# Optimization experiments

Hardware: AMD Instinct MI355X
Metric: run time of the kernel (lower is better)

## Reference

```python
import jax, jax.numpy as jnp
import numpy as np

B, N, D, H = 4, 1024, 1024, 16
DH = D // H
NEG_BIG = -2.0**32 + 1.0  # padding value from the torch code


def setup_inputs() -> dict:
    key = jax.random.key(0)
    ks = jax.random.split(key, 12)
    inp = {
        "x": jax.random.normal(ks[0], (B, N, D), dtype=jnp.float32),
        "key_padding_mask": jnp.zeros((B, N), dtype=bool),  # True = padded
        # attention projections (nn.Linear, bias=False): y = x @ W.T
        "Wq": jax.random.normal(ks[1], (D, D), dtype=jnp.float32) * (D ** -0.5),
        "Wk": jax.random.normal(ks[2], (D, D), dtype=jnp.float32) * (D ** -0.5),
        "Wv": jax.random.normal(ks[3], (D, D), dtype=jnp.float32) * (D ** -0.5),
        # FFN
        "W1": jax.random.normal(ks[4], (D, D), dtype=jnp.float32) * (D ** -0.5),
        "b1": jnp.zeros((D,), dtype=jnp.float32),
        "W2": jax.random.normal(ks[5], (D, D), dtype=jnp.float32) * (D ** -0.5),
        "b2": jnp.zeros((D,), dtype=jnp.float32),
        # MaskedLayerNorm params
        "g1": jnp.ones((D,), dtype=jnp.float32),
        "beta1": jnp.zeros((D,), dtype=jnp.float32),
        "g2": jnp.ones((D,), dtype=jnp.float32),
        "beta2": jnp.zeros((D,), dtype=jnp.float32),
    }
    return inp


def masked_layer_norm(x, scale, bias, eps=1e-5):
    mean = jnp.mean(x, axis=-1, keepdims=True)
    var = jnp.mean(jnp.square(x - mean), axis=-1, keepdims=True)
    return (x - mean) * jax.lax.rsqrt(var + eps) * scale + bias


def _to_heads(t):
    # torch: cat(split(t, DH, dim=2), dim=0) -> head-major [H*B, N, DH]
    b, n, d = t.shape
    return t.reshape(b, n, H, DH).transpose(2, 0, 1, 3).reshape(H * b, n, DH)


def _from_heads(t, b):
    # torch: cat(split(t, B, dim=0), dim=2) -> [B, N, D]
    hb, n, dh = t.shape
    return t.reshape(H, b, n, dh).transpose(1, 2, 0, 3).reshape(b, n, H * dh)


def attention(x, key_padding_mask, Wq, Wk, Wv):
    b, n, d = x.shape
    Q = _to_heads(x @ Wq.T)  # (H*B, N, DH)
    K = _to_heads(x @ Wk.T)
    V = _to_heads(x @ Wv.T)

    scores = jnp.einsum("znd,zmd->znm", Q, K) / (DH ** 0.5)  # (H*B, N, N)

    # key masks: sign of sum|K| over feature dim, broadcast over query axis
    key_masks = jnp.sign(jnp.sum(jnp.abs(K), axis=-1))  # (H*B, N)
    scores = jnp.where(key_masks[:, None, :] == 0, jnp.full_like(scores, NEG_BIG), scores)

    # temporal mask, direction == FORWARD: mask[i, j] = (j > i)
    idx = jnp.arange(n)
    attn_mask = idx[None, :] > idx[:, None]  # sw_row > sw_col with ij meshgrid
    scores = scores + (1.0 - attn_mask.astype(scores.dtype)) * -10000.0

    # NOTE: original code calls F.softmax(outputs) with no dim on a 3D tensor;
    # torch's implicit-dim rule selects dim=0 for ndim==3. Replicated faithfully.
    attn = jax.nn.softmax(scores, axis=0)

    query_masks = jnp.sign(jnp.sum(jnp.abs(Q), axis=-1))  # (H*B, N)
    attn = attn * query_masks[:, :, None]
    # dropout p=0.0 -> identity

    out = jnp.einsum("znm,zmd->znd", attn, V)  # (H*B, N, DH)
    out = _from_heads(out, b)  # (B, N, D)
    out = out * (~key_padding_mask)[:, :, None].astype(out.dtype)
    return out


def reference(x, key_padding_mask, Wq, Wk, Wv, W1, b1, W2, b2, g1, beta1, g2, beta2):
    attn_out = attention(x, key_padding_mask, Wq, Wk, Wv)
    h = masked_layer_norm(x + attn_out, g1, beta1)  # layer_norm1
    ff = jax.nn.relu(h @ W1.T + b1) @ W2.T + b2  # fc (dropout p=0)
    valid = (~key_padding_mask)[:, :, None].astype(ff.dtype)
    ff = ff * valid
    out = masked_layer_norm(ff + h, g2, beta2)  # layer_norm2
    out = out * valid
    return out
```

## Files before the change

### kernel.cpp

```cpp
#include <hip/hip_runtime.h>
#include <math.h>

typedef unsigned short u16;
typedef unsigned char  u8;
typedef unsigned int   u32;
typedef __attribute__((ext_vector_type(8))) short bf16x8;
typedef __attribute__((ext_vector_type(4))) float f32x4;

#define NSEQ   1024
#define DMODEL 1024
#define ZTOT   64
#define LOG2E  1.4426950408889634f

typedef const __attribute__((address_space(1))) void* gp1;
typedef __attribute__((address_space(3))) void* lp3;

__device__ __forceinline__ void gload16(const void* g, void* l) {
    __builtin_amdgcn_global_load_lds((gp1)g, (lp3)l, 16, 0, 0);
}

__device__ __forceinline__ u16 f2bf(float f) {
    u32 u = __builtin_bit_cast(u32, f);
    return (u16)((u + 0x7FFFu + ((u >> 16) & 1u)) >> 16);
}

__device__ __forceinline__ u32 cvt_pk_bf16(float a, float b) {
    u32 r;
    asm("v_cvt_pk_bf16_f32 %0, %1, %2" : "=v"(r) : "v"(a), "v"(b));
    return r;
}

__launch_bounds__(256)
__global__ void cvt_bf16(const float* __restrict__ in, u16* __restrict__ out) {
    int i = (blockIdx.x * 256 + threadIdx.x) * 4;
    float4 v = *(const float4*)(in + i);
    uint2 o;
    o.x = cvt_pk_bf16(v.x, v.y);
    o.y = cvt_pk_bf16(v.z, v.w);
    *(uint2*)(out + i) = o;
}

struct P5 { const float* in[5]; u16* out[5]; };
__launch_bounds__(256)
__global__ void cvt_bf16_5(P5 p) {
    int which = blockIdx.x >> 10;
    int blk   = blockIdx.x & 1023;
    int i = (blk * 256 + threadIdx.x) * 4;
    float4 v = *(const float4*)(p.in[which] + i);
    uint2 o;
    o.x = cvt_pk_bf16(v.x, v.y);
    o.y = cvt_pk_bf16(v.z, v.w);
    *(uint2*)(p.out[which] + i) = o;
}

__launch_bounds__(256)
__global__ void rowmask2_bf(const u16* __restrict__ Kh, const u16* __restrict__ Qh,
                            float* __restrict__ km, float* __restrict__ qm) {
    int b = blockIdx.x;
    const u16* T = (b < 256) ? Kh : Qh;
    float* o = (b < 256) ? km : qm;
    int r = (b & 255) * 256 + threadIdx.x;
    const uint4* p = (const uint4*)(T + (size_t)r * 64);
    u32 acc = 0;
    #pragma unroll
    for (int i = 0; i < 8; i++) {
        uint4 q = p[i];
        acc |= (q.x | q.y | q.z | q.w) & 0x7fff7fffu;
    }
    o[r] = acc ? 1.f : 0.f;
}

__launch_bounds__(256)
__global__ void vt_km(u16* __restrict__ Vt, const float* __restrict__ km) {
    int idx = blockIdx.x * 256 + threadIdx.x;
    int e0 = idx * 8;
    int z = e0 >> 16;
    int tok = e0 & 1023;
    float4 ka = *(const float4*)(km + z * 1024 + tok);
    float4 kb = *(const float4*)(km + z * 1024 + tok + 4);
    uint4 v = *(uint4*)(Vt + e0);
    u32 m;
    m = (ka.x != 0.f ? 0x0000FFFFu : 0u) | (ka.y != 0.f ? 0xFFFF0000u : 0u); v.x &= m;
    m = (ka.z != 0.f ? 0x0000FFFFu : 0u) | (ka.w != 0.f ? 0xFFFF0000u : 0u); v.y &= m;
    m = (kb.x != 0.f ? 0x0000FFFFu : 0u) | (kb.y != 0.f ? 0xFFFF0000u : 0u); v.z &= m;
    m = (kb.z != 0.f ? 0x0000FFFFu : 0u) | (kb.w != 0.f ? 0xFFFF0000u : 0u); v.w &= m;
    *(uint4*)(Vt + e0) = v;
}

__launch_bounds__(256)
__global__ void gemm_qkv(const u16* __restrict__ A,
                         const u16* __restrict__ Wq, const u16* __restrict__ Wk,
                         const u16* __restrict__ Wv,
                         u16* __restrict__ Qh, u16* __restrict__ Kh, u16* __restrict__ Vt)
{
    __shared__ __align__(16) u16 lA[2][128 * 32];
    __shared__ __align__(16) u16 lB[2][128 * 32];
    const int tid = threadIdx.x, lane = tid & 63, w = tid >> 6;
    const int frow = lane & 15, koct = lane >> 4;
    const int sel = blockIdx.x >> 3;
    const int col0 = (blockIdx.x & 7) * 128, row0 = blockIdx.y * 128;
    const u16* B = (sel == 0) ? Wq : (sel == 1) ? Wk : Wv;
    const int wrow = (w >> 1) * 64, wcol = (w & 1) * 64;
    f32x4 acc[4][4] = {};

    auto stage = [&](int buf, int k0) {
        #pragma unroll
        for (int i = 0; i < 2; i++) {
            int p = tid + i * 256;
            int row = p >> 2, sl = p & 3, ssl = sl ^ ((row >> 1) & 3);
            gload16(A + (size_t)(row0 + row) * 1024 + k0 + ssl * 8, (char*)lA[buf] + p * 16);
        }
        #pragma unroll
        for (int i = 0; i < 2; i++) {
            int p = tid + i * 256;
            int row = p >> 2, sl = p & 3, ssl = sl ^ ((row >> 1) & 3);
            gload16(B + (size_t)(col0 + row) * 1024 + k0 + ssl * 8, (char*)lB[buf] + p * 16);
        }
    };

    stage(0, 0);
    __syncthreads();
    int buf = 0;
    for (int k0 = 0; k0 < 1024; k0 += 32) {
        if (k0 + 32 < 1024) stage(buf ^ 1, k0 + 32);
        __builtin_amdgcn_s_setprio(1);
        bf16x8 af[4], bf[4];
        #pragma unroll
        for (int i = 0; i < 4; i++) {
            int r = wrow + i * 16 + frow;
            int sl = koct ^ ((r >> 1) & 3);
            af[i] = *(const bf16x8*)((const char*)lA[buf] + r * 64 + sl * 16);
        }
        #pragma unroll
        for (int j = 0; j < 4; j++) {
            int r = wcol + j * 16 + frow;
            int sl = koct ^ ((r >> 1) & 3);
            bf[j] = *(const bf16x8*)((const char*)lB[buf] + r * 64 + sl * 16);
        }
        #pragma unroll
        for (int i = 0; i < 4; i++)
            #pragma unroll
            for (int j = 0; j < 4; j++)
                acc[i][j] = __builtin_amdgcn_mfma_f32_16x16x32_bf16(af[i], bf[j], acc[i][j], 0, 0, 0);
        __builtin_amdgcn_s_setprio(0);
        __syncthreads();
        buf ^= 1;
    }

    if (sel < 2) {
        const float scale = (sel == 0) ? 0.125f * LOG2E : 1.0f;
        u16* outp = (sel == 0) ? Qh : Kh;
        #pragma unroll
        for (int i = 0; i < 4; i++)
            #pragma unroll
            for (int j = 0; j < 4; j++)
                #pragma unroll
                for (int q = 0; q < 4; q++) {
                    int r = row0 + wrow + i * 16 + koct * 4 + q;
                    int c = col0 + wcol + j * 16 + frow;
                    float v = acc[i][j][q] * scale;
                    outp[(size_t)((c >> 6) * 4 + (r >> 10)) * 65536 +
                         (size_t)(r & 1023) * 64 + (c & 63)] = f2bf(v);
                }
    } else {
        #pragma unroll
        for (int i = 0; i < 4; i++) {
            int r0 = row0 + wrow + i * 16 + koct * 4;
            #pragma unroll
            for (int j = 0; j < 4; j++) {
                int c = col0 + wcol + j * 16 + frow;
                int z = (c >> 6) * 4 + (r0 >> 10);
                uint2 pk;
                pk.x = cvt_pk_bf16(acc[i][j][0], acc[i][j][1]);
                pk.y = cvt_pk_bf16(acc[i][j][2], acc[i][j][3]);
                *(uint2*)(Vt + (size_t)z * 65536 + (size_t)(c & 63) * 1024 + (r0 & 1023)) = pk;
            }
        }
    }
}

template <int MODE>
__launch_bounds__(256)
__global__ void gemm_bt(const u16* __restrict__ A, const u16* __restrict__ B,
                        const float* __restrict__ bias, void* __restrict__ outp)
{
    __shared__ __align__(16) u16 lA[2][128 * 64];
    __shared__ __align__(16) u16 lB[2][64 * 64];
    const int tid = threadIdx.x, lane = tid & 63, w = tid >> 6;
    const int frow = lane & 15, koct = lane >> 4;
    const int col0 = blockIdx.x * 64, row0 = blockIdx.y * 128;
    const int wrow = (w >> 1) * 64, wcol = (w & 1) * 32;
    f32x4 acc[4][2] = {};

    auto stage = [&](int buf, int k0) {
        #pragma unroll
        for (int i = 0; i < 4; i++) {
            int p = tid + i * 256;
            int row = p >> 3, sl = p & 7, ssl = sl ^ (row & 7);
            gload16(A + (size_t)(row0 + row) * 1024 + k0 + ssl * 8, (char*)lA[buf] + p * 16);
        }
        #pragma unroll
        for (int i = 0; i < 2; i++) {
            int p = tid + i * 256;
            int row = p >> 3, sl = p & 7, ssl = sl ^ (row & 7);
            gload16(B + (size_t)(col0 + row) * 1024 + k0 + ssl * 8, (char*)lB[buf] + p * 16);
        }
    };

    stage(0, 0);
    __syncthreads();
    int buf = 0;
    for (int k0 = 0; k0 < 1024; k0 += 64) {
        if (k0 + 64 < 1024) stage(buf ^ 1, k0 + 64);
        __builtin_amdgcn_s_setprio(1);
        #pragma unroll
        for (int ks = 0; ks < 2; ks++) {
            bf16x8 af[4], bf2[2];
            #pragma unroll
            for (int i = 0; i < 4; i++) {
                int r = wrow + i * 16 + frow;
                int sl = (ks * 4 + koct) ^ (r & 7);
                af[i] = *(const bf16x8*)((const char*)lA[buf] + r * 128 + sl * 16);
            }
            #pragma unroll
            for (int j = 0; j < 2; j++) {
                int r = wcol + j * 16 + frow;
                int sl = (ks * 4 + koct) ^ (r & 7);
                bf2[j] = *(const bf16x8*)((const char*)lB[buf] + r * 128 + sl * 16);
            }
            #pragma unroll
            for (int i = 0; i < 4; i++)
                #pragma unroll
                for (int j = 0; j < 2; j++)
                    acc[i][j] = __builtin_amdgcn_mfma_f32_16x16x32_bf16(af[i], bf2[j], acc[i][j], 0, 0, 0);
        }
        __builtin_amdgcn_s_setprio(0);
        __syncthreads();
        buf ^= 1;
    }

    #pragma unroll
    for (int i = 0; i < 4; i++)
        #pragma unroll
        for (int j = 0; j < 2; j++)
            #pragma unroll
            for (int q = 0; q < 4; q++) {
                int r = row0 + wrow + i * 16 + koct * 4 + q;
                int c = col0 + wcol + j * 16 + frow;
                float v = acc[i][j][q] + bias[c];
                if constexpr (MODE == 2) {
                    v = fmaxf(v, 0.f);
                    ((u16*)outp)[(size_t)r * 1024 + c] = f2bf(v);
                } else {
                    ((float*)outp)[(size_t)r * 1024 + c] = v;
                }
            }
}

__launch_bounds__(256)
__global__ void attn_pass1(const u16* __restrict__ Qh, const u16* __restrict__ Kh,
                           const float* __restrict__ km, float* __restrict__ partial)
{
    const int bid = blockIdx.x;
    const int mtzg = (bid & 7) * 8 + ((bid >> 3) & 7);
    const int m0 = (mtzg & 15) * 64, zg = mtzg >> 4;
    const int n0 = (bid >> 6) * 64;

    __shared__ __align__(16) u16 lQ[2][64 * 64];
    __shared__ __align__(16) u16 lK[2][64 * 64];
    const int tid = threadIdx.x, lane = tid & 63, w = tid >> 6;
    const int frow = lane & 15, koct = lane >> 4;
    const int wn = (w >> 1) * 32, wm = (w & 1) * 32;
    f32x4 ssum[2][2] = {};

    auto stage = [&](int buf, int z) {
        #pragma unroll
        for (int i = 0; i < 2; i++) {
            int p = tid + i * 256;
            int row = p >> 3, sl = p & 7, ssl = sl ^ (row & 7);
            gload16(Qh + (size_t)(z * NSEQ + n0 + row) * 64 + ssl * 8, (char*)lQ[buf] + p * 16);
            gload16(Kh + (size_t)(z * NSEQ + m0 + row) * 64 + ssl * 8, (char*)lK[buf] + p * 16);
        }
    };

    const int z0 = zg * 16;
    stage(0, z0);
    __syncthreads();
    int buf = 0;
    for (int zi = 0; zi < 16; zi++) {
        const int z = z0 + zi;
        if (zi < 15) stage(buf ^ 1, z + 1);
        f32x4 km4[2];
        #pragma unroll
        for (int j = 0; j < 2; j++)
            km4[j] = *(const f32x4*)(km + z * NSEQ + m0 + wm + j * 16 + koct * 4);
        f32x4 s[2][2] = {};
        __builtin_amdgcn_s_setprio(1);
        #pragma unroll
        for (int ks = 0; ks < 2; ks++) {
            bf16x8 a[2], b2[2];
            #pragma unroll
            for (int i = 0; i < 2; i++) {
                int r = wn + i * 16 + frow;
                int sl = (ks * 4 + koct) ^ (r & 7);
                a[i] = *(const bf16x8*)((const char*)lQ[buf] + r * 128 + sl * 16);
            }
            #pragma unroll
            for (int j = 0; j < 2; j++) {
                int r = wm + j * 16 + frow;
                int sl = (ks * 4 + koct) ^ (r & 7);
                b2[j] = *(const bf16x8*)((const char*)lK[buf] + r * 128 + sl * 16);
            }
            #pragma unroll
            for (int i = 0; i < 2; i++)
                #pragma unroll
                for (int j = 0; j < 2; j++)
                    s[i][j] = __builtin_amdgcn_mfma_f32_16x16x32_bf16(b2[j], a[i], s[i][j], 0, 0, 0);
        }
        __builtin_amdgcn_s_setprio(0);
        #pragma unroll
        for (int j = 0; j < 2; j++)
            #pragma unroll
            for (int i = 0; i < 2; i++)
                #pragma unroll
                for (int q = 0; q < 4; q++)
                    ssum[i][j][q] += __builtin_amdgcn_exp2f(s[i][j][q]) * km4[j][q];
        __syncthreads();
        buf ^= 1;
    }
    #pragma unroll
    for (int i = 0; i < 2; i++)
        #pragma unroll
        for (int j = 0; j < 2; j++) {
            int ng = n0 + wn + i * 16 + frow;
            int mg = m0 + wm + j * 16 + koct * 4;
            *(f32x4*)(partial + (size_t)zg * 1048576 + (size_t)ng * NSEQ + mg) = ssum[i][j];
        }
}

__launch_bounds__(256)
__global__ void sum_inv(const float* __restrict__ p, float* __restrict__ invS) {
    int i = (blockIdx.x * 256 + threadIdx.x) * 4;
    float4 a = *(const float4*)(p + i);
    float4 b = *(const float4*)(p + 1048576 + i);
    float4 c = *(const float4*)(p + 2097152 + i);
    float4 d = *(const float4*)(p + 3145728 + i);
    float4 r;
    float s;
    s = a.x + b.x + c.x + d.x; r.x = s > 0.f ? 1.f / s : 0.f;
    s = a.y + b.y + c.y + d.y; r.y = s > 0.f ? 1.f / s : 0.f;
    s = a.z + b.z + c.z + d.z; r.z = s > 0.f ? 1.f / s : 0.f;
    s = a.w + b.w + c.w + d.w; r.w = s > 0.f ? 1.f / s : 0.f;
    *(float4*)(invS + i) = r;
}

__launch_bounds__(256)
__global__ void attn_pass2(const u16* __restrict__ Qh, const u16* __restrict__ Kh,
                           const u16* __restrict__ Vt,
                           const float* __restrict__ qm, const float* __restrict__ invS,
                           const u8* __restrict__ pad, float* __restrict__ attn)
{
    const int bid = blockIdx.x;
    const int z  = (bid & 7) * 8 + ((bid >> 3) & 7);
    const int n0 = (bid >> 6) * 64;

    __shared__ __align__(16) u16 lK[2][64 * 64];
    __shared__ __align__(16) u16 lV[2][64 * 64];
    __shared__ __align__(16) u16 lP[64 * 64];
    const int tid = threadIdx.x, lane = tid & 63, w = tid >> 6;
    const int frow = lane & 15, koct = lane >> 4;
    const int hh = z >> 2, bb = z & 3;
    const int wrow = w * 16;
    const int nl_row = wrow + frow;
    const size_t inv_base = (size_t)(n0 + nl_row) * NSEQ;

    bf16x8 aq[2];
    #pragma unroll
    for (int ks = 0; ks < 2; ks++)
        aq[ks] = *(const bf16x8*)(Qh + (size_t)(z * NSEQ + n0 + nl_row) * 64 + ks * 32 + koct * 8);

    auto stage = [&](int buf, int m0) {
        #pragma unroll
        for (int i = 0; i < 2; i++) {
            int p = tid + i * 256;
            int row = p >> 3, sl = p & 7, ssl = sl ^ (row & 7);
            gload16(Kh + (size_t)(z * NSEQ + m0 + row) * 64 + ssl * 8, (char*)lK[buf] + p * 16);
            gload16(Vt + (size_t)z * 65536 + (size_t)row * 1024 + m0 + ssl * 8, (char*)lV[buf] + p * 16);
        }
    };

    f32x4 oacc[4] = {};
    f32x4 iv[4];
    #pragma unroll
    for (int j = 0; j < 4; j++)
        iv[j] = *(const f32x4*)(invS + inv_base + j * 16 + koct * 4);
    stage(0, 0);
    __syncthreads();
    int buf = 0;

    for (int mt = 0; mt < 16; mt++) {
        const int m0 = mt * 64;
        if (mt < 15) stage(buf ^ 1, m0 + 64);
        f32x4 ivn[4];
        if (mt < 15) {
            #pragma unroll
            for (int j = 0; j < 4; j++)
                ivn[j] = *(const f32x4*)(invS + inv_base + m0 + 64 + j * 16 + koct * 4);
        }
        f32x4 s[4] = {};
        __builtin_amdgcn_s_setprio(1);
        #pragma unroll
        for (int ks = 0; ks < 2; ks++) {
            bf16x8 kb[4];
            #pragma unroll
            for (int j = 0; j < 4; j++) {
                int r = j * 16 + frow;
                int sl = (ks * 4 + koct) ^ (r & 7);
                kb[j] = *(const bf16x8*)((const char*)lK[buf] + r * 128 + sl * 16);
            }
            #pragma unroll
            for (int j = 0; j < 4; j++)
                s[j] = __builtin_amdgcn_mfma_f32_16x16x32_bf16(kb[j], aq[ks], s[j], 0, 0, 0);
        }
        __builtin_amdgcn_s_setprio(0);
        #pragma unroll
        for (int j = 0; j < 4; j++) {
            float p0 = __builtin_amdgcn_exp2f(s[j][0]) * iv[j][0];
            float p1 = __builtin_amdgcn_exp2f(s[j][1]) * iv[j][1];
            float p2 = __builtin_amdgcn_exp2f(s[j][2]) * iv[j][2];
            float p3 = __builtin_amdgcn_exp2f(s[j][3]) * iv[j][3];
            uint2 pk;
            pk.x = cvt_pk_bf16(p0, p1);
            pk.y = cvt_pk_bf16(p2, p3);
            int slot = (j * 2 + (koct >> 1)) ^ (nl_row & 7);
            *(uint2*)((char*)lP + nl_row * 128 + slot * 16 + (koct & 1) * 8) = pk;
        }
        __builtin_amdgcn_s_setprio(1);
        #pragma unroll
        for (int ks = 0; ks < 2; ks++) {
            int sl = (ks * 4 + koct) ^ (nl_row & 7);
            bf16x8 pa = *(const bf16x8*)((const char*)lP + nl_row * 128 + sl * 16);
            bf16x8 vb[4];
            #pragma unroll
            for (int dj = 0; dj < 4; dj++) {
                int rr = dj * 16 + frow;
                int sv = (ks * 4 + koct) ^ (rr & 7);
                vb[dj] = *(const bf16x8*)((const char*)lV[buf] + rr * 128 + sv * 16);
            }
            #pragma unroll
            for (int dj = 0; dj < 4; dj++)
                oacc[dj] = __builtin_amdgcn_mfma_f32_16x16x32_bf16(pa, vb[dj], oacc[dj], 0, 0, 0);
        }
        __builtin_amdgcn_s_setprio(0);
        __syncthreads();
        buf ^= 1;
        #pragma unroll
        for (int j = 0; j < 4; j++) iv[j] = ivn[j];
    }

    #pragma unroll
    for (int q = 0; q < 4; q++) {
        int ns = n0 + wrow + koct * 4 + q;
        float f = qm[z * NSEQ + ns] * (pad[bb * NSEQ + ns] ? 0.f : 1.f);
        #pragma unroll
        for (int dj = 0; dj < 4; dj++) {
            int d = dj * 16 + frow;
            attn[(size_t)(bb * NSEQ + ns) * DMODEL + hh * 64 + d] = oacc[dj][q] * f;
        }
    }
}

__launch_bounds__(256)
__global__ void ln_kernel(const float* __restrict__ A, const float* __restrict__ Bv,
                          const float* __restrict__ g, const float* __restrict__ beta,
                          const u8* __restrict__ pad, int mode,
                          float* __restrict__ out, u16* __restrict__ outb)
{
    const int row = blockIdx.x, tid = threadIdx.x;
    const int lane = tid & 63, wv = tid >> 6;
    const float valid = pad[row] ? 0.f : 1.f;
    __shared__ float red[4];

    float4 va = *(const float4*)(A + (size_t)row * 1024 + tid * 4);
    float4 vb = *(const float4*)(Bv + (size_t)row * 1024 + tid * 4);
    float v[4];
    if (mode == 0) {
        v[0] = va.x + vb.x; v[1] = va.y + vb.y; v[2] = va.z + vb.z; v[3] = va.w + vb.w;
    } else {
        v[0] = va.x * valid + vb.x; v[1] = va.y * valid + vb.y;
        v[2] = va.z * valid + vb.z; v[3] = va.w * valid + vb.w;
    }
    float s = v[0] + v[1] + v[2] + v[3];
    #pragma unroll
    for (int off = 32; off > 0; off >>= 1) s += __shfl_down(s, off, 64);
    if (lane == 0) red[wv] = s;
    __syncthreads();
    float mean = (red[0] + red[1] + red[2] + red[3]) * (1.f / 1024.f);
    float sq = 0.f;
    #pragma unroll
    for (int k = 0; k < 4; k++) { float d = v[k] - mean; sq += d * d; }
    __syncthreads();
    #pragma unroll
    for (int off = 32; off > 0; off >>= 1) sq += __shfl_down(sq, off, 64);
    if (lane == 0) red[wv] = sq;
    __syncthreads();
    float var = (red[0] + red[1] + red[2] + red[3]) * (1.f / 1024.f);
    float rstd = rsqrtf(var + 1e-5f);
    float osc = (mode == 0) ? 1.f : valid;
    #pragma unroll
    for (int k = 0; k < 4; k++) {
        int c = tid * 4 + k;
        float o = ((v[k] - mean) * rstd * g[c] + beta[c]) * osc;
        out[(size_t)row * 1024 + c] = o;
        if (outb) outb[(size_t)row * 1024 + c] = f2bf(o);
    }
}

extern "C" void kernel_launch(void* const* d_in, const int* in_sizes, int n_in,
                              void* d_out, int out_size, void* d_ws, size_t ws_size,
                              hipStream_t stream)
{
    const float* x   = (const float*)d_in[0];
    const u8*    pad = (const u8*)d_in[1];
    const float* Wq  = (const float*)d_in[2];
    const float* Wk  = (const float*)d_in[3];
    const float* Wv  = (const float*)d_in[4];
    const float* W1  = (const float*)d_in[5];
    const float* b1  = (const float*)d_in[6];
    const float* W2  = (const float*)d_in[7];
    const float* b2  = (const float*)d_in[8];
    const float* g1  = (const float*)d_in[9];
    const float* be1 = (const float*)d_in[10];
    const float* g2  = (const float*)d_in[11];
    const float* be2 = (const float*)d_in[12];
    float* out = (float*)d_out;

    u16* xb   = (u16*)d_ws;
    u16* Wqb  = xb   + 4194304;
    u16* Wkb  = Wqb  + 1048576;
    u16* Wvb  = Wkb  + 1048576;
    u16* W1b  = Wvb  + 1048576;
    u16* W2b  = W1b  + 1048576;
    u16* Qh   = W2b  + 1048576;
    u16* Kh   = Qh   + 4194304;
    u16* Vt   = Kh   + 4194304;
    u16* hb   = Vt   + 4194304;
    u16* ff1b = hb   + 4194304;
    float* km      = (float*)(ff1b + 4194304);
    float* qm      = km      + 65536;
    float* partial = qm      + 65536;
    float* invS    = partial + 4194304;
    float* h       = invS    + 1048576;

    cvt_bf16<<<4096, 256, 0, stream>>>(x, xb);
    P5 p5;
    p5.in[0] = Wq; p5.in[1] = Wk; p5.in[2] = Wv; p5.in[3] = W1; p5.in[4] = W2;
    p5.out[0] = Wqb; p5.out[1] = Wkb; p5.out[2] = Wvb; p5.out[3] = W1b; p5.out[4] = W2b;
    cvt_bf16_5<<<5120, 256, 0, stream>>>(p5);

    gemm_qkv<<<dim3(24, 32), 256, 0, stream>>>(xb, Wqb, Wkb, Wvb, Qh, Kh, Vt);

    rowmask2_bf<<<512, 256, 0, stream>>>(Kh, Qh, km, qm);
    vt_km<<<4096, 256, 0, stream>>>(Vt, km);

    attn_pass1<<<1024, 256, 0, stream>>>(Qh, Kh, km, partial);
    sum_inv<<<1024, 256, 0, stream>>>(partial, invS);
    attn_pass2<<<1024, 256, 0, stream>>>(Qh, Kh, Vt, qm, invS, pad, out);

    ln_kernel<<<4096, 256, 0, stream>>>(x, out, g1, be1, pad, 0, h, hb);

    gemm_bt<2><<<dim3(16, 32), 256, 0, stream>>>(hb,   W1b, b1, ff1b);
    gemm_bt<3><<<dim3(16, 32), 256, 0, stream>>>(ff1b, W2b, b2, out);

    ln_kernel<<<4096, 256, 0, stream>>>(out, h, g2, be2, pad, 1, out, nullptr);
}
```

Baseline: 200.2 us.

## Drop LDS staging in attention passes; give each wave independent tiles

Both attention passes stop staging Q/K/V tiles through shared memory with double buffering and block barriers. Instead, each wave reads its MFMA operands straight from global memory (relying on L1/L2) and owns its own 32x32 score tile (pass1) or 32-query tile (pass2, which now uses 512 blocks and a per-wave P buffer). The goal is to remove barrier stalls and LDS traffic and to let waves run independently. The cost is more global/L2 load traffic, since operands are no longer shared between the waves of a block, and unswizzled direct loads that may be less coalesced.

```diff
diff --git a/kernel.cpp b/kernel.cpp
--- a/kernel.cpp
+++ b/kernel.cpp
@@ -261,63 +261,42 @@
 __global__ void attn_pass1(const u16* __restrict__ Qh, const u16* __restrict__ Kh,
                            const float* __restrict__ km, float* __restrict__ partial)
 {
-    const int bid = blockIdx.x;
-    const int mtzg = (bid & 7) * 8 + ((bid >> 3) & 7);
-    const int m0 = (mtzg & 15) * 64, zg = mtzg >> 4;
-    const int n0 = (bid >> 6) * 64;
-
-    __shared__ __align__(16) u16 lQ[2][64 * 64];
-    __shared__ __align__(16) u16 lK[2][64 * 64];
     const int tid = threadIdx.x, lane = tid & 63, w = tid >> 6;
     const int frow = lane & 15, koct = lane >> 4;
-    const int wn = (w >> 1) * 32, wm = (w & 1) * 32;
+    const int bid = blockIdx.x;
+    const int c = bid & 7;
+    const int local = (bid >> 3) * 4 + w;
+    const int zg = c >> 1;
+    const int m0 = ((c & 1) * 16 + (local & 15)) * 32;
+    const int n0 = (local >> 4) * 32;
+
     f32x4 ssum[2][2] = {};
-
-    auto stage = [&](int buf, int z) {
-        #pragma unroll
-        for (int i = 0; i < 2; i++) {
-            int p = tid + i * 256;
-            int row = p >> 3, sl = p & 7, ssl = sl ^ (row & 7);
-            gload16(Qh + (size_t)(z * NSEQ + n0 + row) * 64 + ssl * 8, (char*)lQ[buf] + p * 16);
-            gload16(Kh + (size_t)(z * NSEQ + m0 + row) * 64 + ssl * 8, (char*)lK[buf] + p * 16);
-        }
-    };
-
     const int z0 = zg * 16;
-    stage(0, z0);
-    __syncthreads();
-    int buf = 0;
-    for (int zi = 0; zi < 16; zi++) {
-        const int z = z0 + zi;
-        if (zi < 15) stage(buf ^ 1, z + 1);
-        f32x4 km4[2];
-        #pragma unroll
-        for (int j = 0; j < 2; j++)
-            km4[j] = *(const f32x4*)(km + z * NSEQ + m0 + wm + j * 16 + koct * 4);
+    for (int z = z0; z < z0 + 16; z++) {
+        const u16* Qz = Qh + (size_t)z * 65536;
+        const u16* Kz = Kh + (size_t)z * 65536;
         f32x4 s[2][2] = {};
         __builtin_amdgcn_s_setprio(1);
         #pragma unroll
         for (int ks = 0; ks < 2; ks++) {
-            bf16x8 a[2], b2[2];
-            #pragma unroll
-            for (int i = 0; i < 2; i++) {
-                int r = wn + i * 16 + frow;
-                int sl = (ks * 4 + koct) ^ (r & 7);
-                a[i] = *(const bf16x8*)((const char*)lQ[buf] + r * 128 + sl * 16);
-            }
-            #pragma unroll
-            for (int j = 0; j < 2; j++) {
-                int r = wm + j * 16 + frow;
-                int sl = (ks * 4 + koct) ^ (r & 7);
-                b2[j] = *(const bf16x8*)((const char*)lK[buf] + r * 128 + sl * 16);
-            }
+            bf16x8 a[2], kb[2];
+            #pragma unroll
+            for (int i = 0; i < 2; i++)
+                a[i] = *(const bf16x8*)(Qz + (size_t)(n0 + i * 16 + frow) * 64 + ks * 32 + koct * 8);
+            #pragma unroll
+            for (int j = 0; j < 2; j++)
+                kb[j] = *(const bf16x8*)(Kz + (size_t)(m0 + j * 16 + frow) * 64 + ks * 32 + koct * 8);
             #pragma unroll
             for (int i = 0; i < 2; i++)
                 #pragma unroll
                 for (int j = 0; j < 2; j++)
-                    s[i][j] = __builtin_amdgcn_mfma_f32_16x16x32_bf16(b2[j], a[i], s[i][j], 0, 0, 0);
+                    s[i][j] = __builtin_amdgcn_mfma_f32_16x16x32_bf16(kb[j], a[i], s[i][j], 0, 0, 0);
         }
         __builtin_amdgcn_s_setprio(0);
+        f32x4 km4[2];
+        #pragma unroll
+        for (int j = 0; j < 2; j++)
+            km4[j] = *(const f32x4*)(km + z * NSEQ + m0 + j * 16 + koct * 4);
         #pragma unroll
         for (int j = 0; j < 2; j++)
             #pragma unroll
@@ -325,15 +304,13 @@
                 #pragma unroll
                 for (int q = 0; q < 4; q++)
                     ssum[i][j][q] += __builtin_amdgcn_exp2f(s[i][j][q]) * km4[j][q];
-        __syncthreads();
-        buf ^= 1;
     }
     #pragma unroll
     for (int i = 0; i < 2; i++)
         #pragma unroll
         for (int j = 0; j < 2; j++) {
-            int ng = n0 + wn + i * 16 + frow;
-            int mg = m0 + wm + j * 16 + koct * 4;
+            int ng = n0 + i * 16 + frow;
+            int mg = m0 + j * 16 + koct * 4;
             *(f32x4*)(partial + (size_t)zg * 1048576 + (size_t)ng * NSEQ + mg) = ssum[i][j];
         }
 }
@@ -360,114 +337,97 @@
                            const float* __restrict__ qm, const float* __restrict__ invS,
                            const u8* __restrict__ pad, float* __restrict__ attn)
 {
-    const int bid = blockIdx.x;
-    const int z  = (bid & 7) * 8 + ((bid >> 3) & 7);
-    const int n0 = (bid >> 6) * 64;
-
-    __shared__ __align__(16) u16 lK[2][64 * 64];
-    __shared__ __align__(16) u16 lV[2][64 * 64];
-    __shared__ __align__(16) u16 lP[64 * 64];
+    __shared__ __align__(16) u16 lP[4][32 * 64];
     const int tid = threadIdx.x, lane = tid & 63, w = tid >> 6;
     const int frow = lane & 15, koct = lane >> 4;
+    const int bid = blockIdx.x;
+    const int local = (bid >> 3) * 4 + w;
+    const int z  = (bid & 7) * 8 + (local >> 5);
+    const int n0 = (local & 31) * 32;
     const int hh = z >> 2, bb = z & 3;
-    const int wrow = w * 16;
-    const int nl_row = wrow + frow;
-    const size_t inv_base = (size_t)(n0 + nl_row) * NSEQ;
-
-    bf16x8 aq[2];
-    #pragma unroll
-    for (int ks = 0; ks < 2; ks++)
-        aq[ks] = *(const bf16x8*)(Qh + (size_t)(z * NSEQ + n0 + nl_row) * 64 + ks * 32 + koct * 8);
-
-    auto stage = [&](int buf, int m0) {
-        #pragma unroll
-        for (int i = 0; i < 2; i++) {
-            int p = tid + i * 256;
-            int row = p >> 3, sl = p & 7, ssl = sl ^ (row & 7);
-            gload16(Kh + (size_t)(z * NSEQ + m0 + row) * 64 + ssl * 8, (char*)lK[buf] + p * 16);
-            gload16(Vt + (size_t)z * 65536 + (size_t)row * 1024 + m0 + ssl * 8, (char*)lV[buf] + p * 16);
-        }
-    };
-
-    f32x4 oacc[4] = {};
-    f32x4 iv[4];
-    #pragma unroll
-    for (int j = 0; j < 4; j++)
-        iv[j] = *(const f32x4*)(invS + inv_base + j * 16 + koct * 4);
-    stage(0, 0);
-    __syncthreads();
-    int buf = 0;
+    char* lPw = (char*)&lP[w][0];
+
+    const u16* Kz = Kh + (size_t)z * 65536;
+    const u16* Vz = Vt + (size_t)z * 65536;
+
+    bf16x8 aq[2][2];
+    #pragma unroll
+    for (int i = 0; i < 2; i++)
+        #pragma unroll
+        for (int ks = 0; ks < 2; ks++)
+            aq[i][ks] = *(const bf16x8*)(Qh + (size_t)z * 65536 +
+                                         (size_t)(n0 + i * 16 + frow) * 64 + ks * 32 + koct * 8);
+
+    f32x4 oacc[2][4] = {};
 
     for (int mt = 0; mt < 16; mt++) {
         const int m0 = mt * 64;
-        if (mt < 15) stage(buf ^ 1, m0 + 64);
-        f32x4 ivn[4];
-        if (mt < 15) {
-            #pragma unroll
-            for (int j = 0; j < 4; j++)
-                ivn[j] = *(const f32x4*)(invS + inv_base + m0 + 64 + j * 16 + koct * 4);
-        }
-        f32x4 s[4] = {};
+        f32x4 s[2][4] = {};
         __builtin_amdgcn_s_setprio(1);
         #pragma unroll
         for (int ks = 0; ks < 2; ks++) {
             bf16x8 kb[4];
             #pragma unroll
+            for (int j = 0; j < 4; j++)
+                kb[j] = *(const bf16x8*)(Kz + (size_t)(m0 + j * 16 + frow) * 64 + ks * 32 + koct * 8);
+            #pragma unroll
+            for (int i = 0; i < 2; i++)
+                #pragma unroll
+                for (int j = 0; j < 4; j++)
+                    s[i][j] = __builtin_amdgcn_mfma_f32_16x16x32_bf16(kb[j], aq[i][ks], s[i][j], 0, 0, 0);
+        }
+        __builtin_amdgcn_s_setprio(0);
+        #pragma unroll
+        for (int i = 0; i < 2; i++) {
+            const size_t inv_base = (size_t)(n0 + i * 16 + frow) * NSEQ;
+            const int r = i * 16 + frow;
+            #pragma unroll
             for (int j = 0; j < 4; j++) {
-                int r = j * 16 + frow;
+                int mg = m0 + j * 16 + koct * 4;
+                f32x4 iv = *(const f32x4*)(invS + inv_base + mg);
+                float p0 = __builtin_amdgcn_exp2f(s[i][j][0]) * iv[0];
+                float p1 = __builtin_amdgcn_exp2f(s[i][j][1]) * iv[1];
+                float p2 = __builtin_amdgcn_exp2f(s[i][j][2]) * iv[2];
+                float p3 = __builtin_amdgcn_exp2f(s[i][j][3]) * iv[3];
+                uint2 pk;
+                pk.x = cvt_pk_bf16(p0, p1);
+                pk.y = cvt_pk_bf16(p2, p3);
+                int slot = (j * 2 + (koct >> 1)) ^ (r & 7);
+                *(uint2*)(lPw + r * 128 + slot * 16 + (koct & 1) * 8) = pk;
+            }
+        }
+        __builtin_amdgcn_s_setprio(1);
+        #pragma unroll
+        for (int ks = 0; ks < 2; ks++) {
+            bf16x8 vb[4];
+            #pragma unroll
+            for (int dj = 0; dj < 4; dj++)
+                vb[dj] = *(const bf16x8*)(Vz + (size_t)(dj * 16 + frow) * 1024 + m0 + ks * 32 + koct * 8);
+            #pragma unroll
+            for (int i = 0; i < 2; i++) {
+                const int r = i * 16 + frow;
                 int sl = (ks * 4 + koct) ^ (r & 7);
-                kb[j] = *(const bf16x8*)((const char*)lK[buf] + r * 128 + sl * 16);
-            }
-            #pragma unroll
-            for (int j = 0; j < 4; j++)
-                s[j] = __builtin_amdgcn_mfma_f32_16x16x32_bf16(kb[j], aq[ks], s[j], 0, 0, 0);
+                bf16x8 pa = *(const bf16x8*)(lPw + r * 128 + sl * 16);
+                #pragma unroll
+                for (int dj = 0; dj < 4; dj++)
+                    oacc[i][dj] = __builtin_amdgcn_mfma_f32_16x16x32_bf16(pa, vb[dj], oacc[i][dj], 0, 0, 0);
+            }
         }
         __builtin_amdgcn_s_setprio(0);
-        #pragma unroll
-        for (int j = 0; j < 4; j++) {
-            float p0 = __builtin_amdgcn_exp2f(s[j][0]) * iv[j][0];
-            float p1 = __builtin_amdgcn_exp2f(s[j][1]) * iv[j][1];
-            float p2 = __builtin_amdgcn_exp2f(s[j][2]) * iv[j][2];
-            float p3 = __builtin_amdgcn_exp2f(s[j][3]) * iv[j][3];
-            uint2 pk;
-            pk.x = cvt_pk_bf16(p0, p1);
-            pk.y = cvt_pk_bf16(p2, p3);
-            int slot = (j * 2 + (koct >> 1)) ^ (nl_row & 7);
-            *(uint2*)((char*)lP + nl_row * 128 + slot * 16 + (koct & 1) * 8) = pk;
-        }
-        __builtin_amdgcn_s_setprio(1);
-        #pragma unroll
-        for (int ks = 0; ks < 2; ks++) {
-            int sl = (ks * 4 + koct) ^ (nl_row & 7);
-            bf16x8 pa = *(const bf16x8*)((const char*)lP + nl_row * 128 + sl * 16);
-            bf16x8 vb[4];
+    }
+
+    #pragma unroll
+    for (int i = 0; i < 2; i++)
+        #pragma unroll
+        for (int q = 0; q < 4; q++) {
+            int ns = n0 + i * 16 + koct * 4 + q;
+            float f = qm[z * NSEQ + ns] * (pad[bb * NSEQ + ns] ? 0.f : 1.f);
             #pragma unroll
             for (int dj = 0; dj < 4; dj++) {
-                int rr = dj * 16 + frow;
-                int sv = (ks * 4 + koct) ^ (rr & 7);
-                vb[dj] = *(const bf16x8*)((const char*)lV[buf] + rr * 128 + sv * 16);
-            }
-            #pragma unroll
-            for (int dj = 0; dj < 4; dj++)
-                oacc[dj] = __builtin_amdgcn_mfma_f32_16x16x32_bf16(pa, vb[dj], oacc[dj], 0, 0, 0);
-        }
-        __builtin_amdgcn_s_setprio(0);
-        __syncthreads();
-        buf ^= 1;
-        #pragma unroll
-        for (int j = 0; j < 4; j++) iv[j] = ivn[j];
-    }
-
-    #pragma unroll
-    for (int q = 0; q < 4; q++) {
-        int ns = n0 + wrow + koct * 4 + q;
-        float f = qm[z * NSEQ + ns] * (pad[bb * NSEQ + ns] ? 0.f : 1.f);
-        #pragma unroll
-        for (int dj = 0; dj < 4; dj++) {
-            int d = dj * 16 + frow;
-            attn[(size_t)(bb * NSEQ + ns) * DMODEL + hh * 64 + d] = oacc[dj][q] * f;
-        }
-    }
+                int d = dj * 16 + frow;
+                attn[(size_t)(bb * NSEQ + ns) * DMODEL + hh * 64 + d] = oacc[i][dj][q] * f;
+            }
+        }
 }
 
 __launch_bounds__(256)
@@ -565,7 +525,7 @@
 
     attn_pass1<<<1024, 256, 0, stream>>>(Qh, Kh, km, partial);
     sum_inv<<<1024, 256, 0, stream>>>(partial, invS);
-    attn_pass2<<<1024, 256, 0, stream>>>(Qh, Kh, Vt, qm, invS, pad, out);
+    attn_pass2<<<512, 256, 0, stream>>>(Qh, Kh, Vt, qm, invS, pad, out);
 
     ln_kernel<<<4096, 256, 0, stream>>>(x, out, g1, be1, pad, 0, h, hb);
 
```

New measurement: 281.7 us. +40.7%, slower.

## Software-pipeline attention pass2 with smaller key tiles and deferred PV MFMA

Applied to the files above, without the earlier changes.

Restructures attn_pass2 to use 32-key tiles instead of 64, with per-wave double-buffered P tiles. The P·V MFMA for the previous tile is deferred into the next iteration so it overlaps the QK computation and global staging of the following tile. Explicit vmcnt waits and raw s_barriers replace __syncthreads, and the invS loads now happen inline rather than being prefetched a tile ahead. This cuts LDS use and aims to hide load latency, at the cost of twice as many loop iterations and barriers, plus exposed invS global-load latency.

```diff
diff --git a/kernel.cpp b/kernel.cpp
--- a/kernel.cpp
+++ b/kernel.cpp
@@ -360,102 +360,108 @@
                            const float* __restrict__ qm, const float* __restrict__ invS,
                            const u8* __restrict__ pad, float* __restrict__ attn)
 {
+    __shared__ __align__(16) u16 lK[2][32 * 64];
+    __shared__ __align__(16) u16 lV[2][64 * 32];
+    __shared__ __align__(16) u16 lP[2][4][16 * 32];
+    const int tid = threadIdx.x, lane = tid & 63, w = tid >> 6;
+    const int frow = lane & 15, koct = lane >> 4;
     const int bid = blockIdx.x;
     const int z  = (bid & 7) * 8 + ((bid >> 3) & 7);
     const int n0 = (bid >> 6) * 64;
-
-    __shared__ __align__(16) u16 lK[2][64 * 64];
-    __shared__ __align__(16) u16 lV[2][64 * 64];
-    __shared__ __align__(16) u16 lP[64 * 64];
-    const int tid = threadIdx.x, lane = tid & 63, w = tid >> 6;
-    const int frow = lane & 15, koct = lane >> 4;
     const int hh = z >> 2, bb = z & 3;
     const int wrow = w * 16;
     const int nl_row = wrow + frow;
     const size_t inv_base = (size_t)(n0 + nl_row) * NSEQ;
 
+    const u16* Kz = Kh + (size_t)z * 65536;
+    const u16* Vz = Vt + (size_t)z * 65536;
+
     bf16x8 aq[2];
     #pragma unroll
     for (int ks = 0; ks < 2; ks++)
-        aq[ks] = *(const bf16x8*)(Qh + (size_t)(z * NSEQ + n0 + nl_row) * 64 + ks * 32 + koct * 8);
+        aq[ks] = *(const bf16x8*)(Qh + (size_t)z * 65536 +
+                                  (size_t)(n0 + nl_row) * 64 + ks * 32 + koct * 8);
 
     auto stage = [&](int buf, int m0) {
-        #pragma unroll
-        for (int i = 0; i < 2; i++) {
-            int p = tid + i * 256;
-            int row = p >> 3, sl = p & 7, ssl = sl ^ (row & 7);
-            gload16(Kh + (size_t)(z * NSEQ + m0 + row) * 64 + ssl * 8, (char*)lK[buf] + p * 16);
-            gload16(Vt + (size_t)z * 65536 + (size_t)row * 1024 + m0 + ssl * 8, (char*)lV[buf] + p * 16);
+        {
+            int p = tid, row = p >> 3, sl = p & 7, ssl = sl ^ (row & 7);
+            gload16(Kz + (size_t)(m0 + row) * 64 + ssl * 8, (char*)lK[buf] + p * 16);
+        }
+        {
+            int p = tid, row = p >> 2, sl = p & 3, ssl = sl ^ (row & 3);
+            gload16(Vz + (size_t)row * 1024 + m0 + ssl * 8, (char*)lV[buf] + p * 16);
         }
     };
 
     f32x4 oacc[4] = {};
-    f32x4 iv[4];
-    #pragma unroll
-    for (int j = 0; j < 4; j++)
-        iv[j] = *(const f32x4*)(invS + inv_base + j * 16 + koct * 4);
     stage(0, 0);
-    __syncthreads();
-    int buf = 0;
-
-    for (int mt = 0; mt < 16; mt++) {
-        const int m0 = mt * 64;
-        if (mt < 15) stage(buf ^ 1, m0 + 64);
-        f32x4 ivn[4];
-        if (mt < 15) {
-            #pragma unroll
-            for (int j = 0; j < 4; j++)
-                ivn[j] = *(const f32x4*)(invS + inv_base + m0 + 64 + j * 16 + koct * 4);
-        }
-        f32x4 s[4] = {};
+    int buf = 0, pb = 0;
+
+    for (int mt = 0; mt < 32; mt++) {
+        if (mt > 0) {
+            const char* lPw = (const char*)&lP[pb ^ 1][w][0];
+            bf16x8 pa = *(const bf16x8*)(lPw + frow * 64 + koct * 16);
+            __builtin_amdgcn_s_setprio(1);
+            #pragma unroll
+            for (int dj = 0; dj < 4; dj++) {
+                int r = dj * 16 + frow;
+                int slot = koct ^ (r & 3);
+                bf16x8 vb = *(const bf16x8*)((const char*)lV[buf ^ 1] + r * 64 + slot * 16);
+                oacc[dj] = __builtin_amdgcn_mfma_f32_16x16x32_bf16(pa, vb, oacc[dj], 0, 0, 0);
+            }
+            __builtin_amdgcn_s_setprio(0);
+        }
+        __builtin_amdgcn_s_barrier();
+        if (mt < 31) {
+            stage(buf ^ 1, (mt + 1) * 32);
+            asm volatile("s_waitcnt vmcnt(2)" ::: "memory");
+        } else {
+            asm volatile("s_waitcnt vmcnt(0)" ::: "memory");
+        }
+        __builtin_amdgcn_sched_barrier(0);
+        __builtin_amdgcn_s_barrier();
+        const int m0 = mt * 32;
+        f32x4 s[2] = {};
         __builtin_amdgcn_s_setprio(1);
         #pragma unroll
         for (int ks = 0; ks < 2; ks++) {
-            bf16x8 kb[4];
-            #pragma unroll
-            for (int j = 0; j < 4; j++) {
+            #pragma unroll
+            for (int j = 0; j < 2; j++) {
                 int r = j * 16 + frow;
-                int sl = (ks * 4 + koct) ^ (r & 7);
-                kb[j] = *(const bf16x8*)((const char*)lK[buf] + r * 128 + sl * 16);
-            }
-            #pragma unroll
-            for (int j = 0; j < 4; j++)
-                s[j] = __builtin_amdgcn_mfma_f32_16x16x32_bf16(kb[j], aq[ks], s[j], 0, 0, 0);
+                int slot = (ks * 4 + koct) ^ (r & 7);
+                bf16x8 kb = *(const bf16x8*)((const char*)lK[buf] + r * 128 + slot * 16);
+                s[j] = __builtin_amdgcn_mfma_f32_16x16x32_bf16(kb, aq[ks], s[j], 0, 0, 0);
+            }
         }
         __builtin_amdgcn_s_setprio(0);
-        #pragma unroll
-        for (int j = 0; j < 4; j++) {
-            float p0 = __builtin_amdgcn_exp2f(s[j][0]) * iv[j][0];
-            float p1 = __builtin_amdgcn_exp2f(s[j][1]) * iv[j][1];
-            float p2 = __builtin_amdgcn_exp2f(s[j][2]) * iv[j][2];
-            float p3 = __builtin_amdgcn_exp2f(s[j][3]) * iv[j][3];
-            uint2 pk;
-            pk.x = cvt_pk_bf16(p0, p1);
-            pk.y = cvt_pk_bf16(p2, p3);
-            int slot = (j * 2 + (koct >> 1)) ^ (nl_row & 7);
-            *(uint2*)((char*)lP + nl_row * 128 + slot * 16 + (koct & 1) * 8) = pk;
-        }
-        __builtin_amdgcn_s_setprio(1);
-        #pragma unroll
-        for (int ks = 0; ks < 2; ks++) {
-            int sl = (ks * 4 + koct) ^ (nl_row & 7);
-            bf16x8 pa = *(const bf16x8*)((const char*)lP + nl_row * 128 + sl * 16);
-            bf16x8 vb[4];
-            #pragma unroll
-            for (int dj = 0; dj < 4; dj++) {
-                int rr = dj * 16 + frow;
-                int sv = (ks * 4 + koct) ^ (rr & 7);
-                vb[dj] = *(const bf16x8*)((const char*)lV[buf] + rr * 128 + sv * 16);
-            }
-            #pragma unroll
-            for (int dj = 0; dj < 4; dj++)
-                oacc[dj] = __builtin_amdgcn_mfma_f32_16x16x32_bf16(pa, vb[dj], oacc[dj], 0, 0, 0);
-        }
-        __builtin_amdgcn_s_setprio(0);
-        __syncthreads();
-        buf ^= 1;
-        #pragma unroll
-        for (int j = 0; j < 4; j++) iv[j] = ivn[j];
+        {
+            char* lPw = (char*)&lP[pb][w][0];
+            #pragma unroll
+            for (int j = 0; j < 2; j++) {
+                int mg = m0 + j * 16 + koct * 4;
+                f32x4 iv = *(const f32x4*)(invS + inv_base + mg);
+                float p0 = __builtin_amdgcn_exp2f(s[j][0]) * iv[0];
+                float p1 = __builtin_amdgcn_exp2f(s[j][1]) * iv[1];
+                float p2 = __builtin_amdgcn_exp2f(s[j][2]) * iv[2];
+                float p3 = __builtin_amdgcn_exp2f(s[j][3]) * iv[3];
+                uint2 pk;
+                pk.x = cvt_pk_bf16(p0, p1);
+                pk.y = cvt_pk_bf16(p2, p3);
+                *(uint2*)(lPw + frow * 64 + j * 32 + koct * 8) = pk;
+            }
+        }
+        buf ^= 1; pb ^= 1;
+    }
+    {
+        const char* lPw = (const char*)&lP[pb ^ 1][w][0];
+        bf16x8 pa = *(const bf16x8*)(lPw + frow * 64 + koct * 16);
+        #pragma unroll
+        for (int dj = 0; dj < 4; dj++) {
+            int r = dj * 16 + frow;
+            int slot = koct ^ (r & 3);
+            bf16x8 vb = *(const bf16x8*)((const char*)lV[buf ^ 1] + r * 64 + slot * 16);
+            oacc[dj] = __builtin_amdgcn_mfma_f32_16x16x32_bf16(pa, vb, oacc[dj], 0, 0, 0);
+        }
     }
 
     #pragma unroll
```

Result: no change. 202.8 us (+1.3%).

## Single-buffer 128-key tiles in attn_pass2 and merge bf16 conversion kernels

Applied to the files above, without the earlier changes.

The attention pass-2 kernel drops double-buffered 64-key K/V tiles in favour of a single 128-key tile, loaded synchronously between barriers and processed in two 64-wide halves with a per-wave P buffer. This halves the number of barrier iterations and lets each wave write and read its own P slice. The trade-off is that global loads no longer overlap with compute. Separately, the two fp32-to-bf16 conversion kernels are merged into one launch to save a kernel launch.

```diff
diff --git a/kernel.cpp b/kernel.cpp
--- a/kernel.cpp
+++ b/kernel.cpp
@@ -30,27 +30,26 @@
     return r;
 }
 
-__launch_bounds__(256)
-__global__ void cvt_bf16(const float* __restrict__ in, u16* __restrict__ out) {
-    int i = (blockIdx.x * 256 + threadIdx.x) * 4;
+struct P5 { const float* in[5]; u16* out[5]; };
+__launch_bounds__(256)
+__global__ void cvt_all(const float* __restrict__ x, u16* __restrict__ xb, P5 p) {
+    int bid = blockIdx.x;
+    const float* in;
+    u16* out;
+    int blk;
+    if (bid < 4096) { in = x; out = xb; blk = bid; }
+    else {
+        int which = (bid - 4096) >> 10;
+        blk = bid & 1023;
+        in = p.in[which];
+        out = p.out[which];
+    }
+    int i = (blk * 256 + threadIdx.x) * 4;
     float4 v = *(const float4*)(in + i);
     uint2 o;
     o.x = cvt_pk_bf16(v.x, v.y);
     o.y = cvt_pk_bf16(v.z, v.w);
     *(uint2*)(out + i) = o;
-}
-
-struct P5 { const float* in[5]; u16* out[5]; };
-__launch_bounds__(256)
-__global__ void cvt_bf16_5(P5 p) {
-    int which = blockIdx.x >> 10;
-    int blk   = blockIdx.x & 1023;
-    int i = (blk * 256 + threadIdx.x) * 4;
-    float4 v = *(const float4*)(p.in[which] + i);
-    uint2 o;
-    o.x = cvt_pk_bf16(v.x, v.y);
-    o.y = cvt_pk_bf16(v.z, v.w);
-    *(uint2*)(p.out[which] + i) = o;
 }
 
 __launch_bounds__(256)
@@ -360,102 +359,116 @@
                            const float* __restrict__ qm, const float* __restrict__ invS,
                            const u8* __restrict__ pad, float* __restrict__ attn)
 {
+    __shared__ __align__(16) u16 lK[128 * 64];
+    __shared__ __align__(16) u16 lV[64 * 128];
+    __shared__ __align__(16) u16 lP[4][16 * 64];
+    const int tid = threadIdx.x, lane = tid & 63, w = tid >> 6;
+    const int frow = lane & 15, koct = lane >> 4;
     const int bid = blockIdx.x;
     const int z  = (bid & 7) * 8 + ((bid >> 3) & 7);
     const int n0 = (bid >> 6) * 64;
-
-    __shared__ __align__(16) u16 lK[2][64 * 64];
-    __shared__ __align__(16) u16 lV[2][64 * 64];
-    __shared__ __align__(16) u16 lP[64 * 64];
-    const int tid = threadIdx.x, lane = tid & 63, w = tid >> 6;
-    const int frow = lane & 15, koct = lane >> 4;
     const int hh = z >> 2, bb = z & 3;
     const int wrow = w * 16;
-    const int nl_row = wrow + frow;
-    const size_t inv_base = (size_t)(n0 + nl_row) * NSEQ;
+    const size_t inv_base = (size_t)(n0 + wrow + frow) * NSEQ;
+    char* lPw = (char*)&lP[w][0];
+
+    const u16* Kz = Kh + (size_t)z * 65536;
+    const u16* Vz = Vt + (size_t)z * 65536;
 
     bf16x8 aq[2];
     #pragma unroll
     for (int ks = 0; ks < 2; ks++)
-        aq[ks] = *(const bf16x8*)(Qh + (size_t)(z * NSEQ + n0 + nl_row) * 64 + ks * 32 + koct * 8);
-
-    auto stage = [&](int buf, int m0) {
-        #pragma unroll
-        for (int i = 0; i < 2; i++) {
+        aq[ks] = *(const bf16x8*)(Qh + (size_t)z * 65536 +
+                                  (size_t)(n0 + wrow + frow) * 64 + ks * 32 + koct * 8);
+
+    auto stage = [&](int m0) {
+        #pragma unroll
+        for (int i = 0; i < 4; i++) {
             int p = tid + i * 256;
             int row = p >> 3, sl = p & 7, ssl = sl ^ (row & 7);
-            gload16(Kh + (size_t)(z * NSEQ + m0 + row) * 64 + ssl * 8, (char*)lK[buf] + p * 16);
-            gload16(Vt + (size_t)z * 65536 + (size_t)row * 1024 + m0 + ssl * 8, (char*)lV[buf] + p * 16);
+            gload16(Kz + (size_t)(m0 + row) * 64 + ssl * 8, (char*)lK + p * 16);
+        }
+        #pragma unroll
+        for (int i = 0; i < 4; i++) {
+            int p = tid + i * 256;
+            int row = p >> 4, sl = p & 15, ssl = sl ^ (row & 15);
+            gload16(Vz + (size_t)row * 1024 + m0 + ssl * 8, (char*)lV + p * 16);
         }
     };
 
     f32x4 oacc[4] = {};
-    f32x4 iv[4];
+    f32x4 ivA[4], ivB[4];
     #pragma unroll
     for (int j = 0; j < 4; j++)
-        iv[j] = *(const f32x4*)(invS + inv_base + j * 16 + koct * 4);
-    stage(0, 0);
-    __syncthreads();
-    int buf = 0;
-
-    for (int mt = 0; mt < 16; mt++) {
-        const int m0 = mt * 64;
-        if (mt < 15) stage(buf ^ 1, m0 + 64);
-        f32x4 ivn[4];
-        if (mt < 15) {
-            #pragma unroll
-            for (int j = 0; j < 4; j++)
-                ivn[j] = *(const f32x4*)(invS + inv_base + m0 + 64 + j * 16 + koct * 4);
-        }
-        f32x4 s[4] = {};
-        __builtin_amdgcn_s_setprio(1);
-        #pragma unroll
-        for (int ks = 0; ks < 2; ks++) {
-            bf16x8 kb[4];
+        ivA[j] = *(const f32x4*)(invS + inv_base + j * 16 + koct * 4);
+    stage(0);
+    asm volatile("s_waitcnt vmcnt(0)" ::: "memory");
+    __builtin_amdgcn_sched_barrier(0);
+    __builtin_amdgcn_s_barrier();
+
+    for (int mt = 0; mt < 8; mt++) {
+        const int m0 = mt * 128;
+        #pragma unroll
+        for (int j = 0; j < 4; j++)
+            ivB[j] = *(const f32x4*)(invS + inv_base + m0 + 64 + j * 16 + koct * 4);
+
+        #pragma unroll
+        for (int half = 0; half < 2; half++) {
+            f32x4 s[4] = {};
+            __builtin_amdgcn_s_setprio(1);
+            #pragma unroll
+            for (int ks = 0; ks < 2; ks++) {
+                bf16x8 kb[4];
+                #pragma unroll
+                for (int j = 0; j < 4; j++) {
+                    int r = half * 64 + j * 16 + frow;
+                    int sl = (ks * 4 + koct) ^ (r & 7);
+                    kb[j] = *(const bf16x8*)((const char*)lK + r * 128 + sl * 16);
+                }
+                #pragma unroll
+                for (int j = 0; j < 4; j++)
+                    s[j] = __builtin_amdgcn_mfma_f32_16x16x32_bf16(kb[j], aq[ks], s[j], 0, 0, 0);
+            }
+            __builtin_amdgcn_s_setprio(0);
+            if (half == 1 && mt < 7) {
+                #pragma unroll
+                for (int j = 0; j < 4; j++)
+                    ivA[j] = *(const f32x4*)(invS + inv_base + m0 + 128 + j * 16 + koct * 4);
+            }
             #pragma unroll
             for (int j = 0; j < 4; j++) {
-                int r = j * 16 + frow;
-                int sl = (ks * 4 + koct) ^ (r & 7);
-                kb[j] = *(const bf16x8*)((const char*)lK[buf] + r * 128 + sl * 16);
-            }
-            #pragma unroll
-            for (int j = 0; j < 4; j++)
-                s[j] = __builtin_amdgcn_mfma_f32_16x16x32_bf16(kb[j], aq[ks], s[j], 0, 0, 0);
-        }
-        __builtin_amdgcn_s_setprio(0);
-        #pragma unroll
-        for (int j = 0; j < 4; j++) {
-            float p0 = __builtin_amdgcn_exp2f(s[j][0]) * iv[j][0];
-            float p1 = __builtin_amdgcn_exp2f(s[j][1]) * iv[j][1];
-            float p2 = __builtin_amdgcn_exp2f(s[j][2]) * iv[j][2];
-            float p3 = __builtin_amdgcn_exp2f(s[j][3]) * iv[j][3];
-            uint2 pk;
-            pk.x = cvt_pk_bf16(p0, p1);
-            pk.y = cvt_pk_bf16(p2, p3);
-            int slot = (j * 2 + (koct >> 1)) ^ (nl_row & 7);
-            *(uint2*)((char*)lP + nl_row * 128 + slot * 16 + (koct & 1) * 8) = pk;
-        }
-        __builtin_amdgcn_s_setprio(1);
-        #pragma unroll
-        for (int ks = 0; ks < 2; ks++) {
-            int sl = (ks * 4 + koct) ^ (nl_row & 7);
-            bf16x8 pa = *(const bf16x8*)((const char*)lP + nl_row * 128 + sl * 16);
-            bf16x8 vb[4];
-            #pragma unroll
-            for (int dj = 0; dj < 4; dj++) {
-                int rr = dj * 16 + frow;
-                int sv = (ks * 4 + koct) ^ (rr & 7);
-                vb[dj] = *(const bf16x8*)((const char*)lV[buf] + rr * 128 + sv * 16);
-            }
-            #pragma unroll
-            for (int dj = 0; dj < 4; dj++)
-                oacc[dj] = __builtin_amdgcn_mfma_f32_16x16x32_bf16(pa, vb[dj], oacc[dj], 0, 0, 0);
-        }
-        __builtin_amdgcn_s_setprio(0);
-        __syncthreads();
-        buf ^= 1;
-        #pragma unroll
-        for (int j = 0; j < 4; j++) iv[j] = ivn[j];
+                f32x4 iv = half ? ivB[j] : ivA[j];
+                float p0 = __builtin_amdgcn_exp2f(s[j][0]) * iv[0];
+                float p1 = __builtin_amdgcn_exp2f(s[j][1]) * iv[1];
+                float p2 = __builtin_amdgcn_exp2f(s[j][2]) * iv[2];
+                float p3 = __builtin_amdgcn_exp2f(s[j][3]) * iv[3];
+                uint2 pk;
+                pk.x = cvt_pk_bf16(p0, p1);
+                pk.y = cvt_pk_bf16(p2, p3);
+                int slot = (j * 2 + (koct >> 1)) ^ (frow & 7);
+                *(uint2*)(lPw + frow * 128 + slot * 16 + (koct & 1) * 8) = pk;
+            }
+            __builtin_amdgcn_s_setprio(1);
+            #pragma unroll
+            for (int ks = 0; ks < 2; ks++) {
+                int slp = (ks * 4 + koct) ^ (frow & 7);
+                bf16x8 pa = *(const bf16x8*)(lPw + frow * 128 + slp * 16);
+                #pragma unroll
+                for (int dj = 0; dj < 4; dj++) {
+                    int r = dj * 16 + frow;
+                    int s0 = half * 8 + ks * 4 + koct;
+                    int sv = s0 ^ (r & 15);
+                    bf16x8 vb = *(const bf16x8*)((const char*)lV + r * 256 + sv * 16);
+                    oacc[dj] = __builtin_amdgcn_mfma_f32_16x16x32_bf16(pa, vb, oacc[dj], 0, 0, 0);
+                }
+            }
+            __builtin_amdgcn_s_setprio(0);
+        }
+        __builtin_amdgcn_s_barrier();
+        if (mt < 7) stage(m0 + 128);
+        asm volatile("s_waitcnt vmcnt(0)" ::: "memory");
+        __builtin_amdgcn_sched_barrier(0);
+        __builtin_amdgcn_s_barrier();
     }
 
     #pragma unroll
@@ -552,11 +565,10 @@
     float* invS    = partial + 4194304;
     float* h       = invS    + 1048576;
 
-    cvt_bf16<<<4096, 256, 0, stream>>>(x, xb);
     P5 p5;
     p5.in[0] = Wq; p5.in[1] = Wk; p5.in[2] = Wv; p5.in[3] = W1; p5.in[4] = W2;
     p5.out[0] = Wqb; p5.out[1] = Wkb; p5.out[2] = Wvb; p5.out[3] = W1b; p5.out[4] = W2b;
-    cvt_bf16_5<<<5120, 256, 0, stream>>>(p5);
+    cvt_all<<<9216, 256, 0, stream>>>(x, xb, p5);
 
     gemm_qkv<<<dim3(24, 32), 256, 0, stream>>>(xb, Wqb, Wkb, Wvb, Qh, Kh, Vt);
 
```

New measurement: 202.4 us. Within noise of the previous version (+1.1%).
